# Performance work log

Hardware: AMD Instinct MI355X
Metric: run time of the kernel (lower is better)

Reference implementation:

```python
import jax, jax.numpy as jnp
import numpy as np

B, S, D, H = 2, 2048, 1024, 16
HD = D // H
NUM_BUCKETS, MAX_DISTANCE = 32, 128


def setup_inputs() -> dict:
    key = jax.random.key(0)
    ks = jax.random.split(key, 6)
    scale = D ** -0.5
    x = jax.random.normal(ks[0], (B, S, D), dtype=jnp.float32)
    Wq = jax.random.normal(ks[1], (D, D), dtype=jnp.float32) * scale
    Wk = jax.random.normal(ks[2], (D, D), dtype=jnp.float32) * scale
    Wv = jax.random.normal(ks[3], (D, D), dtype=jnp.float32) * scale
    Wo = jax.random.normal(ks[4], (D, D), dtype=jnp.float32) * scale
    rel_emb = jax.random.normal(ks[5], (NUM_BUCKETS, H), dtype=jnp.float32) * 0.02
    # causal mask: True where masked (strictly upper triangular)
    causal_mask = jnp.triu(jnp.ones((S, S), dtype=bool), k=1)
    padding_mask = jnp.zeros((B, S), dtype=bool)  # no PAD tokens
    return {"x": x, "causal_mask": causal_mask, "padding_mask": padding_mask,
            "Wq": Wq, "Wk": Wk, "Wv": Wv, "Wo": Wo, "rel_emb": rel_emb}


def _relative_position_bucket(seq_len: int) -> jnp.ndarray:
    # T5-style bucketing; relative_position = memory - context, n = abs(-rel)
    pos = jnp.arange(seq_len)
    rel = pos[None, :] - pos[:, None]          # (S, S)
    n = jnp.abs(rel)
    max_exact = NUM_BUCKETS // 2
    is_small = n < max_exact
    nf = jnp.maximum(n, 1).astype(jnp.float32)  # avoid log(0); masked by where
    val_if_large = max_exact + (
        jnp.log(nf / max_exact) / np.log(MAX_DISTANCE / max_exact)
        * (NUM_BUCKETS - max_exact)
    ).astype(jnp.int32)
    val_if_large = jnp.minimum(val_if_large, NUM_BUCKETS - 1)
    return jnp.where(is_small, n, val_if_large)


def reference(x, causal_mask, padding_mask, Wq, Wk, Wv, Wo, rel_emb):
    bsz, seq_len, _ = x.shape
    # torch Linear: y = x @ W.T
    q = (x @ Wq.T).reshape(bsz, seq_len, H, HD).transpose(0, 2, 1, 3)
    k = (x @ Wk.T).reshape(bsz, seq_len, H, HD).transpose(0, 2, 1, 3)
    v = (x @ Wv.T).reshape(bsz, seq_len, H, HD).transpose(0, 2, 1, 3)

    scores = jnp.einsum('bhqd,bhkd->bhqk', q, k) / np.sqrt(HD)  # (B,H,S,S)

    buckets = _relative_position_bucket(seq_len)                # (S,S) int
    bias = rel_emb[buckets].transpose(2, 0, 1)[None]            # (1,H,S,S)
    scores = scores + bias

    neg_inf = jnp.array(-jnp.inf, dtype=scores.dtype)
    scores = jnp.where(causal_mask[None, None, :, :], neg_inf, scores)
    scores = jnp.where(padding_mask[:, None, None, :], neg_inf, scores)

    attn = jax.nn.softmax(scores, axis=-1)
    out = jnp.einsum('bhqk,bhkd->bhqd', attn, v)                # (B,H,S,HD)
    out = out.transpose(0, 2, 1, 3).reshape(bsz, seq_len, D)
    return out @ Wo.T
```

## Files before the change

kernel.cpp:

```cpp
#include <hip/hip_runtime.h>
#include <math.h>

#define S_LEN 2048
#define DMODEL 1024
#define NHEAD 16
#define HEADD 64
#define BATCH 2
#define MROWS (BATCH * S_LEN)

typedef __attribute__((ext_vector_type(8))) short bf16x8;
typedef __attribute__((ext_vector_type(4))) float f32x4;
typedef __attribute__((ext_vector_type(4))) unsigned short u16x4;

__device__ __forceinline__ unsigned short f2bf(float f) {
  unsigned int u = __float_as_uint(f);
  u += 0x7fffu + ((u >> 16) & 1u);
  return (unsigned short)(u >> 16);
}

__device__ __forceinline__ void gload_lds16(const void* g, void* l) {
  __builtin_amdgcn_global_load_lds(
      (const __attribute__((address_space(1))) unsigned int*)g,
      (__attribute__((address_space(3))) unsigned int*)l, 16, 0, 0);
}

__global__ void cvt_kernel(const float* __restrict__ src,
                           unsigned short* __restrict__ dst, int n4) {
  int i = blockIdx.x * blockDim.x + threadIdx.x;
  if (i < n4) {
    float4 v = ((const float4*)src)[i];
    u16x4 o;
    o.x = f2bf(v.x); o.y = f2bf(v.y); o.z = f2bf(v.z); o.w = f2bf(v.w);
    ((u16x4*)dst)[i] = o;
  }
}

__global__ void bias_kernel(const float* __restrict__ rel_emb,
                            float* __restrict__ bias) {
  int i = blockIdx.x * blockDim.x + threadIdx.x;
  if (i >= NHEAD * S_LEN) return;
  int d = i & (S_LEN - 1);
  int h = i >> 11;
  int bucket;
  if (d < 16) {
    bucket = d;
  } else {
    float t = logf((float)d * 0.0625f) / 2.0794415416798357f * 16.0f;
    bucket = 16 + (int)t;
    if (bucket > 31) bucket = 31;
  }
  bias[h * S_LEN + d] = rel_emb[bucket * NHEAD + h];
}

template <typename OT, int MREP>
__global__ __launch_bounds__(256, 2)
void gemm_bt(const unsigned short* __restrict__ A,
             const unsigned short* __restrict__ B0,
             const unsigned short* __restrict__ B1,
             const unsigned short* __restrict__ B2,
             OT* __restrict__ C0, OT* __restrict__ C1, OT* __restrict__ C2,
             int M, int N, int K) {
  constexpr int BM = MREP * 32;
  __shared__ unsigned short As[2][BM * 32];
  __shared__ unsigned short Bs[2][128 * 32];
  const unsigned short* Bt = (blockIdx.z == 0) ? B0 : (blockIdx.z == 1 ? B1 : B2);
  OT* C = (blockIdx.z == 0) ? C0 : (blockIdx.z == 1 ? C1 : C2);
  const int tid = threadIdx.x;
  const int w = tid >> 6, l = tid & 63;
  const int g = l >> 4, c = l & 15;
  const int m0 = blockIdx.y * BM, n0 = blockIdx.x * 128;
  const int wr = (w >> 1) * (BM / 2), wc = (w & 1) * 64;

  f32x4 acc[MREP][4] = {};

  auto stage = [&](int k0, int bu) {
#pragma unroll
    for (int it = 0; it < MREP / 2; ++it) {
      int ti = it * 256 + tid;
      int row = ti >> 2, ch = ti & 3;
      gload_lds16(A + (size_t)(m0 + row) * K + k0 + ch * 8,
                  (char*)As[bu] + (it * 256 + w * 64) * 16);
    }
#pragma unroll
    for (int it = 0; it < 2; ++it) {
      int ti = it * 256 + tid;
      int row = ti >> 2, ch = ti & 3;
      gload_lds16(Bt + (size_t)(n0 + row) * K + k0 + ch * 8,
                  (char*)Bs[bu] + (it * 256 + w * 64) * 16);
    }
  };

  stage(0, 0);
  for (int k0 = 0; k0 < K; k0 += 32) {
    const int bu = (k0 >> 5) & 1;
    asm volatile("s_waitcnt vmcnt(0)" ::: "memory");
    __builtin_amdgcn_sched_barrier(0);
    __builtin_amdgcn_s_barrier();
    if (k0 + 32 < K) stage(k0 + 32, bu ^ 1);

    bf16x8 af[MREP], bfr[4];
#pragma unroll
    for (int mf = 0; mf < MREP; ++mf)
      af[mf] = *(const bf16x8*)((const char*)As[bu] + (wr + mf * 16 + c) * 64 + g * 16);
#pragma unroll
    for (int nf = 0; nf < 4; ++nf)
      bfr[nf] = *(const bf16x8*)((const char*)Bs[bu] + (wc + nf * 16 + c) * 64 + g * 16);
#pragma unroll
    for (int mf = 0; mf < MREP; ++mf)
#pragma unroll
      for (int nf = 0; nf < 4; ++nf)
        acc[mf][nf] = __builtin_amdgcn_mfma_f32_16x16x32_bf16(
            af[mf], bfr[nf], acc[mf][nf], 0, 0, 0);
  }

#pragma unroll
  for (int mf = 0; mf < MREP; ++mf)
#pragma unroll
    for (int nf = 0; nf < 4; ++nf)
#pragma unroll
      for (int r = 0; r < 4; ++r) {
        int row = m0 + wr + mf * 16 + g * 4 + r;
        int col = n0 + wc + nf * 16 + c;
        float v = acc[mf][nf][r];
        if constexpr (sizeof(OT) == 2)
          C[(size_t)row * N + col] = (OT)f2bf(v);
        else
          C[(size_t)row * N + col] = v;
      }
}

__global__ void vtrans_kernel(const unsigned short* __restrict__ V,
                              unsigned short* __restrict__ Vt) {
  __shared__ unsigned short tl[64][72];
  const int tid = threadIdx.x;
  const int bh = blockIdx.y, b = bh >> 4, h = bh & 15;
  const int s0 = blockIdx.x * 64;
  {
    int r = tid >> 2, cq = (tid & 3) * 16;
    const unsigned short* src =
        V + (size_t)(b * S_LEN + s0 + r) * DMODEL + h * HEADD + cq;
    *(bf16x8*)&tl[r][cq] = *(const bf16x8*)src;
    *(bf16x8*)&tl[r][cq + 8] = *(const bf16x8*)(src + 8);
  }
  __syncthreads();
  {
    int hd = tid >> 2, sq = (tid & 3) * 16;
    unsigned short tmp[16];
#pragma unroll
    for (int j = 0; j < 16; ++j) tmp[j] = tl[sq + j][hd];
    unsigned short* dst = Vt + (size_t)(bh * 64 + hd) * S_LEN + s0 + sq;
    *(bf16x8*)dst = *(const bf16x8*)tmp;
    *(bf16x8*)(dst + 8) = *(const bf16x8*)(tmp + 8);
  }
}

__global__ __launch_bounds__(256, 2)
void attn_kernel(const unsigned short* __restrict__ Q,
                 const unsigned short* __restrict__ K,
                 const unsigned short* __restrict__ Vt,
                 const float* __restrict__ bias,
                 unsigned short* __restrict__ O) {
  __shared__ unsigned short Ks[2][64 * 64];
  __shared__ unsigned short Vs[2][64 * 64];
  __shared__ unsigned short Ps[4][16 * 64];
  __shared__ float bls[S_LEN];
  const int tid = threadIdx.x;
  const int w = tid >> 6, l = tid & 63;
  const int g = l >> 4, c = l & 15;
  const int bh = blockIdx.y, b = bh >> 4, h = bh & 15;
  const unsigned short* Qb = Q + (size_t)b * S_LEN * DMODEL + h * HEADD;
  const unsigned short* Kb = K + (size_t)b * S_LEN * DMODEL + h * HEADD;
  const unsigned short* Vtb = Vt + (size_t)bh * HEADD * S_LEN;

  {
    const float4* src = (const float4*)(bias + h * S_LEN);
    float4* dst = (float4*)bls;
    dst[tid] = src[tid];
    dst[tid + 256] = src[tid + 256];
  }
  __syncthreads();

  auto stage = [&](int kv0, int bu) {
#pragma unroll
    for (int it = 0; it < 2; ++it) {
      int ti = it * 256 + tid;
      int row = ti >> 3, ch = ti & 7;
      int sch = ch ^ (row & 7);
      gload_lds16(Kb + (size_t)(kv0 + row) * DMODEL + sch * 8,
                  (char*)Ks[bu] + (it * 256 + w * 64) * 16);
      gload_lds16(Vtb + (size_t)row * S_LEN + kv0 + sch * 8,
                  (char*)Vs[bu] + (it * 256 + w * 64) * 16);
    }
  };

  const int pi = blockIdx.x;
#pragma unroll 1
  for (int phase = 0; phase < 2; ++phase) {
    const int qt = phase ? (31 - pi) : pi;
    const int q0 = qt * 64;
    const int nt = qt + 1;
    const int wrow0 = q0 + w * 16;

    bf16x8 aq[2];
#pragma unroll
    for (int kh = 0; kh < 2; ++kh)
      aq[kh] = *(const bf16x8*)(Qb + (size_t)(wrow0 + c) * DMODEL + kh * 32 + g * 8);

    f32x4 oacc[4] = {};
    float mst[4], lst[4];
#pragma unroll
    for (int r = 0; r < 4; ++r) { mst[r] = -1e30f; lst[r] = 0.f; }

    __builtin_amdgcn_s_barrier();
    stage(0, 0);

#pragma unroll 1
    for (int t = 0; t < nt; ++t) {
      const int kv0 = t * 64;
      const int bu = t & 1;
      asm volatile("s_waitcnt vmcnt(0)" ::: "memory");
      __builtin_amdgcn_sched_barrier(0);
      __builtin_amdgcn_s_barrier();
      if (t + 1 < nt) stage((t + 1) * 64, bu ^ 1);

      f32x4 sac[4] = {};
#pragma unroll
      for (int kh = 0; kh < 2; ++kh) {
        bf16x8 bk[4];
#pragma unroll
        for (int nf = 0; nf < 4; ++nf) {
          int row = nf * 16 + c;
          int off = (row * 128 + (kh * 4 + g) * 16) ^ ((row & 7) << 4);
          bk[nf] = *(const bf16x8*)((const char*)Ks[bu] + off);
        }
#pragma unroll
        for (int nf = 0; nf < 4; ++nf)
          sac[nf] = __builtin_amdgcn_mfma_f32_16x16x32_bf16(
              aq[kh], bk[nf], sac[nf], 0, 0, 0);
      }
      float p[4][4];
      float mx[4];
#pragma unroll
      for (int r = 0; r < 4; ++r) {
        int row = wrow0 + g * 4 + r;
        float rm = -1e30f;
#pragma unroll
        for (int nf = 0; nf < 4; ++nf) {
          int col = kv0 + nf * 16 + c;
          int d = row - col;
          float bv = bls[d < 0 ? 0 : d];
          float sv = (col <= row) ? sac[nf][r] * 0.125f + bv : -1e30f;
          p[nf][r] = sv;
          rm = fmaxf(rm, sv);
        }
#pragma unroll
        for (int msk = 1; msk < 16; msk <<= 1)
          rm = fmaxf(rm, __shfl_xor(rm, msk));
        mx[r] = rm;
      }
#pragma unroll
      for (int r = 0; r < 4; ++r) {
        float mnew = fmaxf(mst[r], mx[r]);
        float scl = __expf(mst[r] - mnew);
        float rs = 0.f;
#pragma unroll
        for (int nf = 0; nf < 4; ++nf) {
          float pv = __expf(p[nf][r] - mnew);
          p[nf][r] = pv;
          rs += pv;
        }
#pragma unroll
        for (int msk = 1; msk < 16; msk <<= 1)
          rs += __shfl_xor(rs, msk);
        lst[r] = lst[r] * scl + rs;
        mst[r] = mnew;
#pragma unroll
        for (int nh = 0; nh < 4; ++nh) oacc[nh][r] *= scl;
      }
#pragma unroll
      for (int nf = 0; nf < 4; ++nf)
#pragma unroll
        for (int r = 0; r < 4; ++r) {
          int rowl = g * 4 + r;
          int off = (rowl * 128 + (nf * 16 + c) * 2) ^ ((rowl & 7) << 4);
          *(unsigned short*)((char*)Ps[w] + off) = f2bf(p[nf][r]);
        }
#pragma unroll
      for (int kh = 0; kh < 2; ++kh) {
        bf16x8 pa, vb[4];
        {
          int off = (c * 128 + (kh * 4 + g) * 16) ^ ((c & 7) << 4);
          pa = *(const bf16x8*)((const char*)Ps[w] + off);
        }
#pragma unroll
        for (int nh = 0; nh < 4; ++nh) {
          int row = nh * 16 + c;
          int off = (row * 128 + (kh * 4 + g) * 16) ^ ((row & 7) << 4);
          vb[nh] = *(const bf16x8*)((const char*)Vs[bu] + off);
        }
#pragma unroll
        for (int nh = 0; nh < 4; ++nh)
          oacc[nh] = __builtin_amdgcn_mfma_f32_16x16x32_bf16(
              pa, vb[nh], oacc[nh], 0, 0, 0);
      }
    }

#pragma unroll
    for (int nh = 0; nh < 4; ++nh)
#pragma unroll
      for (int r = 0; r < 4; ++r) {
        int row = wrow0 + g * 4 + r;
        int col = h * HEADD + nh * 16 + c;
        O[(size_t)(b * S_LEN + row) * DMODEL + col] =
            f2bf(oacc[nh][r] / lst[r]);
      }
  }
}

extern "C" void kernel_launch(void* const* d_in, const int* in_sizes, int n_in,
                              void* d_out, int out_size, void* d_ws, size_t ws_size,
                              hipStream_t stream) {
  const float* x   = (const float*)d_in[0];
  const float* Wq  = (const float*)d_in[3];
  const float* Wk  = (const float*)d_in[4];
  const float* Wv  = (const float*)d_in[5];
  const float* Wo  = (const float*)d_in[6];
  const float* rel = (const float*)d_in[7];
  float* out = (float*)d_out;

  char* ws = (char*)d_ws;
  const size_t MB = 1u << 20;
  unsigned short* xb  = (unsigned short*)(ws);
  unsigned short* Oa  = xb;
  unsigned short* Qb  = (unsigned short*)(ws + 8 * MB);
  unsigned short* Kb  = (unsigned short*)(ws + 16 * MB);
  unsigned short* Vb  = (unsigned short*)(ws + 24 * MB);
  unsigned short* Vtb = (unsigned short*)(ws + 32 * MB);
  unsigned short* Wqb = (unsigned short*)(ws + 40 * MB);
  unsigned short* Wkb = (unsigned short*)(ws + 42 * MB);
  unsigned short* Wvb = (unsigned short*)(ws + 44 * MB);
  unsigned short* Wob = (unsigned short*)(ws + 46 * MB);
  float* bias = (float*)(ws + 48 * MB);

  cvt_kernel<<<4096, 256, 0, stream>>>(x, xb, 1 << 20);
  cvt_kernel<<<1024, 256, 0, stream>>>(Wq, Wqb, 1 << 18);
  cvt_kernel<<<1024, 256, 0, stream>>>(Wk, Wkb, 1 << 18);
  cvt_kernel<<<1024, 256, 0, stream>>>(Wv, Wvb, 1 << 18);
  cvt_kernel<<<1024, 256, 0, stream>>>(Wo, Wob, 1 << 18);

  bias_kernel<<<128, 256, 0, stream>>>(rel, bias);

  gemm_bt<unsigned short, 4><<<dim3(8, 32, 3), 256, 0, stream>>>(
      xb, Wqb, Wkb, Wvb, Qb, Kb, Vb, MROWS, DMODEL, DMODEL);

  vtrans_kernel<<<dim3(32, 32), 256, 0, stream>>>(Vb, Vtb);

  attn_kernel<<<dim3(16, BATCH * NHEAD), 256, 0, stream>>>(
      Qb, Kb, Vtb, bias, Oa);

  gemm_bt<float, 2><<<dim3(8, 64, 1), 256, 0, stream>>>(
      Oa, Wob, Wob, Wob, out, out, out, MROWS, DMODEL, DMODEL);
}
```

Measured before the change: 254.4 us.

## Restructure attention: smaller query tiles, transposed MFMA softmax, lazy rescale, bf16 bias

The attention kernel now uses 128-thread blocks over 32-row query tiles, doubling the grid, and the QK and PV MFMAs are issued with swapped operands. Each lane therefore owns one query row, so the row max and sum need only two cross-lane shuffles. The running-max rescale is skipped unless the max grows by more than 8, probabilities and outputs are packed with v_cvt_pk_bf16_f32, and the output goes through LDS so rows are stored with coalesced 16-byte writes. The bias table is stored as bf16 and the GEMM launch bound is raised to 3 blocks per CU. Risks include bf16 bias precision, more K/V reloads per query row, and register pressure in the GEMM under the higher occupancy target.

```diff
diff --git a/kernel.cpp b/kernel.cpp
--- a/kernel.cpp
+++ b/kernel.cpp
@@ -16,6 +16,12 @@
   unsigned int u = __float_as_uint(f);
   u += 0x7fffu + ((u >> 16) & 1u);
   return (unsigned short)(u >> 16);
+}
+
+__device__ __forceinline__ unsigned int pk_bf16(float lo, float hi) {
+  unsigned int u;
+  asm("v_cvt_pk_bf16_f32 %0, %1, %2" : "=v"(u) : "v"(lo), "v"(hi));
+  return u;
 }
 
 __device__ __forceinline__ void gload_lds16(const void* g, void* l) {
@@ -36,7 +42,7 @@
 }
 
 __global__ void bias_kernel(const float* __restrict__ rel_emb,
-                            float* __restrict__ bias) {
+                            unsigned short* __restrict__ bias) {
   int i = blockIdx.x * blockDim.x + threadIdx.x;
   if (i >= NHEAD * S_LEN) return;
   int d = i & (S_LEN - 1);
@@ -49,11 +55,11 @@
     bucket = 16 + (int)t;
     if (bucket > 31) bucket = 31;
   }
-  bias[h * S_LEN + d] = rel_emb[bucket * NHEAD + h];
+  bias[h * S_LEN + d] = f2bf(rel_emb[bucket * NHEAD + h]);
 }
 
 template <typename OT, int MREP>
-__global__ __launch_bounds__(256, 2)
+__global__ __launch_bounds__(256, 3)
 void gemm_bt(const unsigned short* __restrict__ A,
              const unsigned short* __restrict__ B0,
              const unsigned short* __restrict__ B1,
@@ -154,16 +160,16 @@
   }
 }
 
-__global__ __launch_bounds__(256, 2)
+__global__ __launch_bounds__(128, 2)
 void attn_kernel(const unsigned short* __restrict__ Q,
                  const unsigned short* __restrict__ K,
                  const unsigned short* __restrict__ Vt,
-                 const float* __restrict__ bias,
+                 const unsigned short* __restrict__ bias,
                  unsigned short* __restrict__ O) {
   __shared__ unsigned short Ks[2][64 * 64];
   __shared__ unsigned short Vs[2][64 * 64];
-  __shared__ unsigned short Ps[4][16 * 64];
-  __shared__ float bls[S_LEN];
+  __shared__ unsigned short Ps[2][16 * 64];
+  __shared__ unsigned short bls[S_LEN];
   const int tid = threadIdx.x;
   const int w = tid >> 6, l = tid & 63;
   const int g = l >> 4, c = l & 15;
@@ -173,43 +179,42 @@
   const unsigned short* Vtb = Vt + (size_t)bh * HEADD * S_LEN;
 
   {
-    const float4* src = (const float4*)(bias + h * S_LEN);
-    float4* dst = (float4*)bls;
+    const bf16x8* src = (const bf16x8*)(bias + h * S_LEN);
+    bf16x8* dst = (bf16x8*)bls;
     dst[tid] = src[tid];
-    dst[tid + 256] = src[tid + 256];
+    dst[tid + 128] = src[tid + 128];
   }
   __syncthreads();
 
   auto stage = [&](int kv0, int bu) {
 #pragma unroll
-    for (int it = 0; it < 2; ++it) {
-      int ti = it * 256 + tid;
+    for (int it = 0; it < 4; ++it) {
+      int ti = it * 128 + tid;
       int row = ti >> 3, ch = ti & 7;
       int sch = ch ^ (row & 7);
       gload_lds16(Kb + (size_t)(kv0 + row) * DMODEL + sch * 8,
-                  (char*)Ks[bu] + (it * 256 + w * 64) * 16);
+                  (char*)Ks[bu] + (it * 128 + w * 64) * 16);
       gload_lds16(Vtb + (size_t)row * S_LEN + kv0 + sch * 8,
-                  (char*)Vs[bu] + (it * 256 + w * 64) * 16);
+                  (char*)Vs[bu] + (it * 128 + w * 64) * 16);
     }
   };
 
   const int pi = blockIdx.x;
 #pragma unroll 1
   for (int phase = 0; phase < 2; ++phase) {
-    const int qt = phase ? (31 - pi) : pi;
-    const int q0 = qt * 64;
-    const int nt = qt + 1;
+    const int qt = phase ? (63 - pi) : pi;
+    const int q0 = qt * 32;
+    const int nt = qt / 2 + 1;
     const int wrow0 = q0 + w * 16;
+    const int qglob = wrow0 + c;
 
     bf16x8 aq[2];
 #pragma unroll
     for (int kh = 0; kh < 2; ++kh)
-      aq[kh] = *(const bf16x8*)(Qb + (size_t)(wrow0 + c) * DMODEL + kh * 32 + g * 8);
+      aq[kh] = *(const bf16x8*)(Qb + (size_t)qglob * DMODEL + kh * 32 + g * 8);
 
     f32x4 oacc[4] = {};
-    float mst[4], lst[4];
-#pragma unroll
-    for (int r = 0; r < 4; ++r) { mst[r] = -1e30f; lst[r] = 0.f; }
+    float mreg = -1e30f, lreg = 0.f;
 
     __builtin_amdgcn_s_barrier();
     stage(0, 0);
@@ -236,84 +241,95 @@
 #pragma unroll
         for (int nf = 0; nf < 4; ++nf)
           sac[nf] = __builtin_amdgcn_mfma_f32_16x16x32_bf16(
-              aq[kh], bk[nf], sac[nf], 0, 0, 0);
-      }
+              bk[nf], aq[kh], sac[nf], 0, 0, 0);
+      }
+
       float p[4][4];
-      float mx[4];
-#pragma unroll
-      for (int r = 0; r < 4; ++r) {
-        int row = wrow0 + g * 4 + r;
-        float rm = -1e30f;
-#pragma unroll
-        for (int nf = 0; nf < 4; ++nf) {
-          int col = kv0 + nf * 16 + c;
-          int d = row - col;
-          float bv = bls[d < 0 ? 0 : d];
-          float sv = (col <= row) ? sac[nf][r] * 0.125f + bv : -1e30f;
+      float pmax = -1e30f;
+#pragma unroll
+      for (int nf = 0; nf < 4; ++nf)
+#pragma unroll
+        for (int r = 0; r < 4; ++r) {
+          int kg = kv0 + nf * 16 + g * 4 + r;
+          int d = qglob - kg;
+          float bv = __uint_as_float((unsigned int)bls[d < 0 ? 0 : d] << 16);
+          float sv = (d >= 0) ? sac[nf][r] * 0.125f + bv : -1e30f;
           p[nf][r] = sv;
-          rm = fmaxf(rm, sv);
-        }
-#pragma unroll
-        for (int msk = 1; msk < 16; msk <<= 1)
-          rm = fmaxf(rm, __shfl_xor(rm, msk));
-        mx[r] = rm;
-      }
-#pragma unroll
-      for (int r = 0; r < 4; ++r) {
-        float mnew = fmaxf(mst[r], mx[r]);
-        float scl = __expf(mst[r] - mnew);
-        float rs = 0.f;
-#pragma unroll
-        for (int nf = 0; nf < 4; ++nf) {
-          float pv = __expf(p[nf][r] - mnew);
+          pmax = fmaxf(pmax, sv);
+        }
+      pmax = fmaxf(pmax, __shfl_xor(pmax, 16));
+      pmax = fmaxf(pmax, __shfl_xor(pmax, 32));
+
+      if (!__all(pmax - mreg <= 8.f)) {
+        float mnew = fmaxf(mreg, pmax);
+        float scl = __expf(mreg - mnew);
+        lreg *= scl;
+#pragma unroll
+        for (int nh = 0; nh < 4; ++nh)
+#pragma unroll
+          for (int r = 0; r < 4; ++r) oacc[nh][r] *= scl;
+        mreg = mnew;
+      }
+      float lsum = 0.f;
+#pragma unroll
+      for (int nf = 0; nf < 4; ++nf)
+#pragma unroll
+        for (int r = 0; r < 4; ++r) {
+          float pv = __expf(p[nf][r] - mreg);
           p[nf][r] = pv;
-          rs += pv;
-        }
-#pragma unroll
-        for (int msk = 1; msk < 16; msk <<= 1)
-          rs += __shfl_xor(rs, msk);
-        lst[r] = lst[r] * scl + rs;
-        mst[r] = mnew;
-#pragma unroll
-        for (int nh = 0; nh < 4; ++nh) oacc[nh][r] *= scl;
-      }
-#pragma unroll
-      for (int nf = 0; nf < 4; ++nf)
-#pragma unroll
-        for (int r = 0; r < 4; ++r) {
-          int rowl = g * 4 + r;
-          int off = (rowl * 128 + (nf * 16 + c) * 2) ^ ((rowl & 7) << 4);
-          *(unsigned short*)((char*)Ps[w] + off) = f2bf(p[nf][r]);
-        }
+          lsum += pv;
+        }
+      lsum += __shfl_xor(lsum, 16);
+      lsum += __shfl_xor(lsum, 32);
+      lreg += lsum;
+
+#pragma unroll
+      for (int nf = 0; nf < 4; ++nf) {
+        unsigned int u0 = pk_bf16(p[nf][0], p[nf][1]);
+        unsigned int u1 = pk_bf16(p[nf][2], p[nf][3]);
+        int off = (c * 128 + nf * 32 + g * 8) ^ ((c & 7) << 4);
+        *(uint2*)((char*)Ps[w] + off) = make_uint2(u0, u1);
+      }
+
 #pragma unroll
       for (int kh = 0; kh < 2; ++kh) {
-        bf16x8 pa, vb[4];
+        bf16x8 pa, va[4];
         {
-          int off = (c * 128 + (kh * 4 + g) * 16) ^ ((c & 7) << 4);
+          int off = (c * 128 + kh * 64 + g * 16) ^ ((c & 7) << 4);
           pa = *(const bf16x8*)((const char*)Ps[w] + off);
         }
 #pragma unroll
         for (int nh = 0; nh < 4; ++nh) {
           int row = nh * 16 + c;
           int off = (row * 128 + (kh * 4 + g) * 16) ^ ((row & 7) << 4);
-          vb[nh] = *(const bf16x8*)((const char*)Vs[bu] + off);
+          va[nh] = *(const bf16x8*)((const char*)Vs[bu] + off);
         }
 #pragma unroll
         for (int nh = 0; nh < 4; ++nh)
           oacc[nh] = __builtin_amdgcn_mfma_f32_16x16x32_bf16(
-              pa, vb[nh], oacc[nh], 0, 0, 0);
-      }
-    }
-
-#pragma unroll
-    for (int nh = 0; nh < 4; ++nh)
-#pragma unroll
-      for (int r = 0; r < 4; ++r) {
-        int row = wrow0 + g * 4 + r;
-        int col = h * HEADD + nh * 16 + c;
-        O[(size_t)(b * S_LEN + row) * DMODEL + col] =
-            f2bf(oacc[nh][r] / lst[r]);
-      }
+              va[nh], pa, oacc[nh], 0, 0, 0);
+      }
+    }
+
+    {
+      float inv = 1.f / lreg;
+#pragma unroll
+      for (int nh = 0; nh < 4; ++nh) {
+        unsigned int u0 = pk_bf16(oacc[nh][0] * inv, oacc[nh][1] * inv);
+        unsigned int u1 = pk_bf16(oacc[nh][2] * inv, oacc[nh][3] * inv);
+        int off = (c * 128 + nh * 32 + g * 8) ^ ((c & 7) << 4);
+        *(uint2*)((char*)Ps[w] + off) = make_uint2(u0, u1);
+      }
+      int rowq = l >> 2, ch2 = l & 3;
+      int off1 = (rowq * 128 + ch2 * 16) ^ ((rowq & 7) << 4);
+      int off2 = (rowq * 128 + (ch2 + 4) * 16) ^ ((rowq & 7) << 4);
+      bf16x8 o1 = *(const bf16x8*)((const char*)Ps[w] + off1);
+      bf16x8 o2 = *(const bf16x8*)((const char*)Ps[w] + off2);
+      unsigned short* orow =
+          O + (size_t)(b * S_LEN + wrow0 + rowq) * DMODEL + h * HEADD;
+      *(bf16x8*)(orow + ch2 * 8) = o1;
+      *(bf16x8*)(orow + (ch2 + 4) * 8) = o2;
+    }
   }
 }
 
@@ -340,7 +356,7 @@
   unsigned short* Wkb = (unsigned short*)(ws + 42 * MB);
   unsigned short* Wvb = (unsigned short*)(ws + 44 * MB);
   unsigned short* Wob = (unsigned short*)(ws + 46 * MB);
-  float* bias = (float*)(ws + 48 * MB);
+  unsigned short* bias = (unsigned short*)(ws + 48 * MB);
 
   cvt_kernel<<<4096, 256, 0, stream>>>(x, xb, 1 << 20);
   cvt_kernel<<<1024, 256, 0, stream>>>(Wq, Wqb, 1 << 18);
@@ -355,7 +371,7 @@
 
   vtrans_kernel<<<dim3(32, 32), 256, 0, stream>>>(Vb, Vtb);
 
-  attn_kernel<<<dim3(16, BATCH * NHEAD), 256, 0, stream>>>(
+  attn_kernel<<<dim3(32, BATCH * NHEAD), 128, 0, stream>>>(
       Qb, Kb, Vtb, bias, Oa);
 
   gemm_bt<float, 2><<<dim3(8, 64, 1), 256, 0, stream>>>(
```

New measurement: 240.6 us. 1.06x faster.
